# Kernel optimization log

Measured on AMD Instinct MI355X. Metric: run time of the kernel, lower is better.

## Reference

```python
import jax, jax.numpy as jnp
import numpy as np

B, S, D, H = 2, 2048, 1024, 16
DK = D // H


def setup_inputs() -> dict:
    key = jax.random.key(0)
    ks = jax.random.split(key, 8)
    scale = 1.0 / np.sqrt(D)
    inp = {
        "query": jax.random.normal(ks[0], (B, S, D), dtype=jnp.float32),
        "key": jax.random.normal(ks[1], (B, S, D), dtype=jnp.float32),
        "value": jax.random.normal(ks[2], (B, S, D), dtype=jnp.float32),
        # causal mask, broadcastable over batch and heads
        "mask": jnp.tril(jnp.ones((S, S), dtype=jnp.int32))[None, None, :, :],
        "W_q": jax.random.normal(ks[3], (D, D), dtype=jnp.float32) * scale,
        "W_k": jax.random.normal(ks[4], (D, D), dtype=jnp.float32) * scale,
        "W_v": jax.random.normal(ks[5], (D, D), dtype=jnp.float32) * scale,
        "W_o": jax.random.normal(ks[6], (D, D), dtype=jnp.float32) * scale,
    }
    return inp


def _split_heads(t):
    Bb, Ss, _ = t.shape
    return t.reshape(Bb, Ss, H, DK).transpose(0, 2, 1, 3)  # [B,H,S,DK]


def reference(query, key, value, mask, W_q, W_k, W_v, W_o):
    # Linear(d,d,bias=False): y = x @ W^T (torch stores weight as [out,in])
    Q = _split_heads(query @ W_q.T)
    K = _split_heads(key @ W_k.T)
    V = _split_heads(value @ W_v.T)
    scores = jnp.einsum("bhqd,bhkd->bhqk", Q, K) / jnp.sqrt(jnp.float32(DK))
    scores = jnp.where(mask == 0, -jnp.inf, scores)
    weights = jax.nn.softmax(scores, axis=-1)
    weights = jnp.nan_to_num(weights, nan=0.0)  # fully-masked rows -> 0
    # dropout is identity at inference
    x = jnp.einsum("bhqk,bhkd->bhqd", weights, V)
    x = x.transpose(0, 2, 1, 3).reshape(B, S, D)
    return x @ W_o.T
```

## Files before the change

### kernel.cpp

```cpp
#include <hip/hip_runtime.h>
#include <hip/hip_bf16.h>

#define D_MODEL 1024
#define NHEAD   16
#define HDK     64
#define SEQ     2048
#define BATCH   2
#define BS      (BATCH * SEQ)

typedef __attribute__((ext_vector_type(8))) short bf16x8;
typedef __attribute__((ext_vector_type(4))) float f32x4;

__device__ __forceinline__ unsigned short f2bf(float f) {
    unsigned u = __builtin_bit_cast(unsigned, f);
    u += 0x7fffu + ((u >> 16) & 1u);
    return (unsigned short)(u >> 16);
}

__device__ __forceinline__ unsigned pk_rne(float x, float y) {
    return (unsigned)f2bf(x) | ((unsigned)f2bf(y) << 16);
}

__device__ __forceinline__ unsigned pack_hi(float x, float y) {
    return __builtin_amdgcn_perm(__builtin_bit_cast(unsigned, y),
                                 __builtin_bit_cast(unsigned, x), 0x07060302u);
}

__device__ __forceinline__ float fexp2(float x) {
#if __has_builtin(__builtin_amdgcn_exp2f)
    return __builtin_amdgcn_exp2f(x);
#else
    return exp2f(x);
#endif
}

typedef const void __attribute__((address_space(1))) gas_void;
typedef void __attribute__((address_space(3))) las_void;

__device__ __forceinline__ void gll16(const void* g, void* l) {
    __builtin_amdgcn_global_load_lds((gas_void*)g, (las_void*)l, 16, 0, 0);
}

template <int ROWS>
__device__ __forceinline__ void stage_f32(const float* __restrict__ X, int ld,
                                          unsigned short* Ls, int t) {
    #pragma unroll
    for (int g = 0; g < ROWS / 32; ++g) {
        int row = (t >> 3) + g * 32;
        int sl  = t & 7;
        int col = (sl ^ (row & 7)) * 8;
        const float4* p = (const float4*)(X + (size_t)row * ld + col);
        float4 a = p[0], b = p[1];
        *(uint4*)&Ls[row * 64 + sl * 8] =
            make_uint4(pk_rne(a.x, a.y), pk_rne(a.z, a.w),
                       pk_rne(b.x, b.y), pk_rne(b.z, b.w));
    }
}

__global__ __launch_bounds__(256)
void proj_gemm(const float* __restrict__ qx, const float* __restrict__ kx,
               const float* __restrict__ vx, const float* __restrict__ wq,
               const float* __restrict__ wk, const float* __restrict__ wv,
               unsigned short* __restrict__ Qp, unsigned short* __restrict__ Kp,
               unsigned short* __restrict__ VT) {
    __shared__ __align__(16) unsigned short As[128 * 64];
    __shared__ __align__(16) unsigned short Bs[128 * 64];

    const int p = blockIdx.z;
    const float* X = p == 0 ? qx : p == 1 ? kx : vx;
    const float* W = p == 0 ? wq : p == 1 ? wk : wv;
    const int bm = blockIdx.y * 128, bn = blockIdx.x * 128;

    const int t    = threadIdx.x;
    const int w    = t >> 6;
    const int L    = t & 63;
    const int quad = L >> 4;
    const int lm   = L & 15;
    const int wr   = (w >> 1) * 64;
    const int wc   = (w & 1) * 64;

    f32x4 acc[4][4];
    #pragma unroll
    for (int ms = 0; ms < 4; ++ms)
        #pragma unroll
        for (int ns = 0; ns < 4; ++ns)
            acc[ms][ns] = (f32x4){0.f, 0.f, 0.f, 0.f};

    for (int kt = 0; kt < D_MODEL; kt += 64) {
        __syncthreads();
        stage_f32<128>(X + (size_t)bm * D_MODEL + kt, D_MODEL, As, t);
        stage_f32<128>(W + (size_t)bn * D_MODEL + kt, D_MODEL, Bs, t);
        __syncthreads();

        #pragma unroll
        for (int ch = 0; ch < 2; ++ch) {
            bf16x8 af[4], bfr[4];
            #pragma unroll
            for (int ms = 0; ms < 4; ++ms) {
                int row = wr + ms * 16 + lm;
                af[ms] = *(const bf16x8*)&As[row * 64 + (((ch * 4 + quad) ^ (row & 7)) * 8)];
            }
            #pragma unroll
            for (int ns = 0; ns < 4; ++ns) {
                int row = wc + ns * 16 + lm;
                bfr[ns] = *(const bf16x8*)&Bs[row * 64 + (((ch * 4 + quad) ^ (row & 7)) * 8)];
            }
            #pragma unroll
            for (int ms = 0; ms < 4; ++ms)
                #pragma unroll
                for (int ns = 0; ns < 4; ++ns)
                    acc[ms][ns] = __builtin_amdgcn_mfma_f32_16x16x32_bf16(
                        af[ms], bfr[ns], acc[ms][ns], 0, 0, 0);
        }
    }

    if (p == 2) {
        const int b    = bm >> 11;
        const int s_in = (bm & (SEQ - 1)) + wr;
        #pragma unroll
        for (int ms = 0; ms < 4; ++ms)
            #pragma unroll
            for (int ns = 0; ns < 4; ++ns) {
                int dg = bn + wc + ns * 16 + lm;
                int h  = dg >> 6, d = dg & 63;
                ushort4 pkv = make_ushort4(f2bf(acc[ms][ns][0]), f2bf(acc[ms][ns][1]),
                                           f2bf(acc[ms][ns][2]), f2bf(acc[ms][ns][3]));
                *(ushort4*)&VT[((size_t)((b * NHEAD + h) * HDK + d)) * SEQ +
                               s_in + ms * 16 + quad * 4] = pkv;
            }
    } else {
        unsigned short* Y = p == 0 ? Qp : Kp;
        const float scl = p == 0 ? 0.18033688011112042f : 1.0f;
        #pragma unroll
        for (int ms = 0; ms < 4; ++ms)
            #pragma unroll
            for (int ns = 0; ns < 4; ++ns)
                #pragma unroll
                for (int r = 0; r < 4; ++r)
                    Y[(size_t)(bm + wr + ms * 16 + quad * 4 + r) * D_MODEL +
                      bn + wc + ns * 16 + lm] = f2bf(acc[ms][ns][r] * scl);
    }
}

__global__ __launch_bounds__(256)
void out_gemm(const unsigned short* __restrict__ X, const float* __restrict__ W,
              float* __restrict__ Y) {
    __shared__ __align__(16) unsigned short As[128 * 64];
    __shared__ __align__(16) unsigned short Bs[64 * 64];
    const int bm = blockIdx.y * 128, bn = blockIdx.x * 64;

    const int t    = threadIdx.x;
    const int w    = t >> 6;
    const int L    = t & 63;
    const int quad = L >> 4;
    const int lm   = L & 15;
    const int r8   = L >> 3;
    const int sl   = L & 7;
    const int xcol = ((sl ^ r8) & 7) * 8;

    f32x4 acc[2][4];
    #pragma unroll
    for (int ms = 0; ms < 2; ++ms)
        #pragma unroll
        for (int ns = 0; ns < 4; ++ns)
            acc[ms][ns] = (f32x4){0.f, 0.f, 0.f, 0.f};

    for (int kt = 0; kt < D_MODEL; kt += 64) {
        __syncthreads();
        #pragma unroll
        for (int i = 0; i < 4; ++i) {
            int c = w * 4 + i;
            gll16(X + (size_t)(bm + c * 8 + r8) * D_MODEL + kt + xcol, &As[c * 512]);
        }
        stage_f32<64>(W + (size_t)bn * D_MODEL + kt, D_MODEL, Bs, t);
        __syncthreads();

        #pragma unroll
        for (int ch = 0; ch < 2; ++ch) {
            bf16x8 af[2], bfr[4];
            #pragma unroll
            for (int ms = 0; ms < 2; ++ms) {
                int row = w * 32 + ms * 16 + lm;
                af[ms] = *(const bf16x8*)&As[row * 64 + (((ch * 4 + quad) ^ (row & 7)) * 8)];
            }
            #pragma unroll
            for (int ns = 0; ns < 4; ++ns) {
                int row = ns * 16 + lm;
                bfr[ns] = *(const bf16x8*)&Bs[row * 64 + (((ch * 4 + quad) ^ (row & 7)) * 8)];
            }
            #pragma unroll
            for (int ms = 0; ms < 2; ++ms)
                #pragma unroll
                for (int ns = 0; ns < 4; ++ns)
                    acc[ms][ns] = __builtin_amdgcn_mfma_f32_16x16x32_bf16(
                        af[ms], bfr[ns], acc[ms][ns], 0, 0, 0);
        }
    }

    #pragma unroll
    for (int ms = 0; ms < 2; ++ms)
        #pragma unroll
        for (int ns = 0; ns < 4; ++ns)
            #pragma unroll
            for (int r = 0; r < 4; ++r)
                Y[(size_t)(bm + w * 32 + ms * 16 + quad * 4 + r) * D_MODEL +
                  bn + ns * 16 + lm] = acc[ms][ns][r];
}

__global__ __launch_bounds__(256)
void attn_mfma(const unsigned short* __restrict__ Q, const unsigned short* __restrict__ K,
               const unsigned short* __restrict__ VT, unsigned short* __restrict__ A) {
    __shared__ __align__(16) unsigned short Ks[2][64 * 72];
    __shared__ __align__(16) unsigned short Vs[2][64 * 72];
    __shared__ __align__(16) unsigned short Ps[4][16 * 72];

    const int t    = threadIdx.x;
    const int w    = t >> 6;
    const int L    = t & 63;
    const int quad = L >> 4;
    const int lm   = L & 15;

    const int f    = blockIdx.x;
    const int qt   = 31 - (f >> 5);
    const int bh   = f & 31;
    const int b    = bh >> 4, h = bh & 15;
    const int q0   = qt * 64;
    const size_t hb  = (size_t)b * SEQ * D_MODEL + h * HDK;
    const size_t vhb = (size_t)(b * NHEAD + h) * HDK;

    const int srow = t >> 2;
    const int sc   = (t & 3) * 16;
    const unsigned short* kp = K + hb + (size_t)srow * D_MODEL + sc;
    const unsigned short* vp = VT + (vhb + srow) * SEQ + sc;
    unsigned short* ps = &Ps[w][0];

    const int qrow = q0 + w * 16 + lm;
    bf16x8 Qf0, Qf1;
    {
        const unsigned short* qp = Q + hb + (size_t)qrow * D_MODEL + quad * 8;
        Qf0 = *(const bf16x8*)qp;
        Qf1 = *(const bf16x8*)(qp + 32);
    }

    f32x4 Oacc[4];
    #pragma unroll
    for (int nt = 0; nt < 4; ++nt) Oacc[nt] = (f32x4){0.f, 0.f, 0.f, 0.f};
    float m_run = -INFINITY, l_part = 0.f;

    float4 k0r = *(const float4*)kp;
    float4 k1r = *(const float4*)(kp + 8);
    float4 v0r = *(const float4*)vp;
    float4 v1r = *(const float4*)(vp + 8);
    *(float4*)&Ks[0][srow * 72 + sc]     = k0r;
    *(float4*)&Ks[0][srow * 72 + sc + 8] = k1r;
    *(float4*)&Vs[0][srow * 72 + sc]     = v0r;
    *(float4*)&Vs[0][srow * 72 + sc + 8] = v1r;
    if (qt >= 1) {
        k0r = *(const float4*)(kp + (size_t)64 * D_MODEL);
        k1r = *(const float4*)(kp + (size_t)64 * D_MODEL + 8);
        v0r = *(const float4*)(vp + 64);
        v1r = *(const float4*)(vp + 64 + 8);
    }
    __syncthreads();

    int bb = 0;
    for (int kt = 0; kt <= qt; ++kt) {
        if (kt < qt) {
            unsigned short* Kn = Ks[bb ^ 1];
            unsigned short* Vn = Vs[bb ^ 1];
            *(float4*)&Kn[srow * 72 + sc]     = k0r;
            *(float4*)&Kn[srow * 72 + sc + 8] = k1r;
            *(float4*)&Vn[srow * 72 + sc]     = v0r;
            *(float4*)&Vn[srow * 72 + sc + 8] = v1r;
            if (kt + 2 <= qt) {
                k0r = *(const float4*)(kp + (size_t)(kt + 2) * 64 * D_MODEL);
                k1r = *(const float4*)(kp + (size_t)(kt + 2) * 64 * D_MODEL + 8);
                v0r = *(const float4*)(vp + (kt + 2) * 64);
                v1r = *(const float4*)(vp + (kt + 2) * 64 + 8);
            }
        }
        const unsigned short* Kc = Ks[bb];
        const unsigned short* Vc = Vs[bb];

        f32x4 S[4];
        #pragma unroll
        for (int ct = 0; ct < 4; ++ct) {
            bf16x8 a0 = *(const bf16x8*)&Kc[(ct * 16 + lm) * 72 + quad * 8];
            bf16x8 a1 = *(const bf16x8*)&Kc[(ct * 16 + lm) * 72 + 32 + quad * 8];
            f32x4 z = (f32x4){0.f, 0.f, 0.f, 0.f};
            z = __builtin_amdgcn_mfma_f32_16x16x32_bf16(a0, Qf0, z, 0, 0, 0);
            z = __builtin_amdgcn_mfma_f32_16x16x32_bf16(a1, Qf1, z, 0, 0, 0);
            S[ct] = z;
        }

        if (kt == qt) {
            #pragma unroll
            for (int ct = 0; ct < 4; ++ct)
                #pragma unroll
                for (int r = 0; r < 4; ++r)
                    if ((q0 + ct * 16 + quad * 4 + r) > qrow)
                        S[ct][r] = -1e30f;
        }

        float m = fmaxf(fmaxf(fmaxf(S[0][0], S[0][1]), fmaxf(S[0][2], S[0][3])),
                        fmaxf(fmaxf(S[1][0], S[1][1]), fmaxf(S[1][2], S[1][3])));
        m = fmaxf(m, fmaxf(fmaxf(fmaxf(S[2][0], S[2][1]), fmaxf(S[2][2], S[2][3])),
                           fmaxf(fmaxf(S[3][0], S[3][1]), fmaxf(S[3][2], S[3][3]))));
        m = fmaxf(m, __shfl_xor(m, 16));
        m = fmaxf(m, __shfl_xor(m, 32));
        const float m_new = fmaxf(m_run, m);
        const float alpha = fexp2(m_run - m_new);
        m_run = m_new;
        float psum = 0.f;
        #pragma unroll
        for (int ct = 0; ct < 4; ++ct)
            #pragma unroll
            for (int r = 0; r < 4; ++r) {
                float e = fexp2(S[ct][r] - m_new);
                S[ct][r] = e;
                psum += e;
            }
        l_part = l_part * alpha + psum;

        #pragma unroll
        for (int ct = 0; ct < 4; ++ct) {
            uint2 pw = make_uint2(pack_hi(S[ct][0], S[ct][1]),
                                  pack_hi(S[ct][2], S[ct][3]));
            *(uint2*)&ps[lm * 72 + ct * 16 + quad * 4] = pw;
        }
        bf16x8 Pb0 = *(const bf16x8*)&ps[lm * 72 + quad * 8];
        bf16x8 Pb1 = *(const bf16x8*)&ps[lm * 72 + 32 + quad * 8];

        #pragma unroll
        for (int nt = 0; nt < 4; ++nt) {
            bf16x8 a0 = *(const bf16x8*)&Vc[(nt * 16 + lm) * 72 + quad * 8];
            bf16x8 a1 = *(const bf16x8*)&Vc[(nt * 16 + lm) * 72 + 32 + quad * 8];
            f32x4 o = Oacc[nt];
            #pragma unroll
            for (int r = 0; r < 4; ++r) o[r] *= alpha;
            o = __builtin_amdgcn_mfma_f32_16x16x32_bf16(a0, Pb0, o, 0, 0, 0);
            o = __builtin_amdgcn_mfma_f32_16x16x32_bf16(a1, Pb1, o, 0, 0, 0);
            Oacc[nt] = o;
        }

        __syncthreads();
        bb ^= 1;
    }

    float l = l_part;
    l += __shfl_xor(l, 16);
    l += __shfl_xor(l, 32);
    const float inv_l = 1.f / l;
    #pragma unroll
    for (int nt = 0; nt < 4; ++nt) {
        ushort4 pkv = make_ushort4(f2bf(Oacc[nt][0] * inv_l), f2bf(Oacc[nt][1] * inv_l),
                                   f2bf(Oacc[nt][2] * inv_l), f2bf(Oacc[nt][3] * inv_l));
        *(ushort4*)&ps[lm * 72 + nt * 16 + quad * 4] = pkv;
    }
    #pragma unroll
    for (int cc = 0; cc < 2; ++cc) {
        int row = cc * 8 + (L >> 3);
        int seg = L & 7;
        uint4 val = *(const uint4*)&ps[row * 72 + seg * 8];
        *(uint4*)&A[hb + (size_t)(q0 + w * 16 + row) * D_MODEL + seg * 8] = val;
    }
}

extern "C" void kernel_launch(void* const* d_in, const int* in_sizes, int n_in,
                              void* d_out, int out_size, void* d_ws, size_t ws_size,
                              hipStream_t stream) {
    const float* q  = (const float*)d_in[0];
    const float* k  = (const float*)d_in[1];
    const float* v  = (const float*)d_in[2];
    const float* Wq = (const float*)d_in[4];
    const float* Wk = (const float*)d_in[5];
    const float* Wv = (const float*)d_in[6];
    const float* Wo = (const float*)d_in[7];
    float* out = (float*)d_out;

    char* ws = (char*)d_ws;
    const size_t MB = 1024 * 1024;
    unsigned short* Qp  = (unsigned short*)(ws + 0 * MB);
    unsigned short* Kp  = (unsigned short*)(ws + 8 * MB);
    unsigned short* VTp = (unsigned short*)(ws + 16 * MB);
    unsigned short* Ap  = (unsigned short*)(ws + 24 * MB);

    proj_gemm<<<dim3(D_MODEL / 128, BS / 128, 3), 256, 0, stream>>>(
        q, k, v, Wq, Wk, Wv, Qp, Kp, VTp);

    attn_mfma<<<dim3(1024), 256, 0, stream>>>(Qp, Kp, VTp, Ap);

    out_gemm<<<dim3(D_MODEL / 64, BS / 128), 256, 0, stream>>>(Ap, Wo, out);
}
```

Before: 255.0 us.

## Pre-cast weights to bf16 and load them via direct-to-LDS; swizzle block order

Adds a kernel that converts all four weight matrices to bf16 once per call into workspace. The projection and output GEMMs then fetch weight tiles with global_load_lds instead of reading fp32 through registers and converting each time. Both GEMMs also move to a 1D grid with a grouped block-index mapping meant to improve L2 reuse. The cost is one extra launch plus an extra pass over the weights, and the workspace layout grows.

```diff
diff --git a/kernel.cpp b/kernel.cpp
--- a/kernel.cpp
+++ b/kernel.cpp
@@ -39,6 +39,20 @@
 
 __device__ __forceinline__ void gll16(const void* g, void* l) {
     __builtin_amdgcn_global_load_lds((gas_void*)g, (las_void*)l, 16, 0, 0);
+}
+
+__global__ __launch_bounds__(256)
+void cast_wt(const float* a, const float* b, const float* c, const float* dd,
+             unsigned short* oa, unsigned short* ob, unsigned short* oc,
+             unsigned short* od) {
+    int i = blockIdx.x * 256 + threadIdx.x;
+    const float* s = blockIdx.y == 0 ? a : blockIdx.y == 1 ? b : blockIdx.y == 2 ? c : dd;
+    unsigned short* d = blockIdx.y == 0 ? oa : blockIdx.y == 1 ? ob : blockIdx.y == 2 ? oc : od;
+    const float4* p = (const float4*)s + (size_t)i * 2;
+    float4 x = p[0], y = p[1];
+    uint4 pk = make_uint4(pk_rne(x.x, x.y), pk_rne(x.z, x.w),
+                          pk_rne(y.x, y.y), pk_rne(y.z, y.w));
+    *((uint4*)d + i) = pk;
 }
 
 template <int ROWS>
@@ -59,95 +73,21 @@
 
 __global__ __launch_bounds__(256)
 void proj_gemm(const float* __restrict__ qx, const float* __restrict__ kx,
-               const float* __restrict__ vx, const float* __restrict__ wq,
-               const float* __restrict__ wk, const float* __restrict__ wv,
+               const float* __restrict__ vx, const unsigned short* __restrict__ wq,
+               const unsigned short* __restrict__ wk, const unsigned short* __restrict__ wv,
                unsigned short* __restrict__ Qp, unsigned short* __restrict__ Kp,
                unsigned short* __restrict__ VT) {
     __shared__ __align__(16) unsigned short As[128 * 64];
     __shared__ __align__(16) unsigned short Bs[128 * 64];
 
-    const int p = blockIdx.z;
-    const float* X = p == 0 ? qx : p == 1 ? kx : vx;
-    const float* W = p == 0 ? wq : p == 1 ? wk : wv;
-    const int bm = blockIdx.y * 128, bn = blockIdx.x * 128;
-
-    const int t    = threadIdx.x;
-    const int w    = t >> 6;
-    const int L    = t & 63;
-    const int quad = L >> 4;
-    const int lm   = L & 15;
-    const int wr   = (w >> 1) * 64;
-    const int wc   = (w & 1) * 64;
-
-    f32x4 acc[4][4];
-    #pragma unroll
-    for (int ms = 0; ms < 4; ++ms)
-        #pragma unroll
-        for (int ns = 0; ns < 4; ++ns)
-            acc[ms][ns] = (f32x4){0.f, 0.f, 0.f, 0.f};
-
-    for (int kt = 0; kt < D_MODEL; kt += 64) {
-        __syncthreads();
-        stage_f32<128>(X + (size_t)bm * D_MODEL + kt, D_MODEL, As, t);
-        stage_f32<128>(W + (size_t)bn * D_MODEL + kt, D_MODEL, Bs, t);
-        __syncthreads();
-
-        #pragma unroll
-        for (int ch = 0; ch < 2; ++ch) {
-            bf16x8 af[4], bfr[4];
-            #pragma unroll
-            for (int ms = 0; ms < 4; ++ms) {
-                int row = wr + ms * 16 + lm;
-                af[ms] = *(const bf16x8*)&As[row * 64 + (((ch * 4 + quad) ^ (row & 7)) * 8)];
-            }
-            #pragma unroll
-            for (int ns = 0; ns < 4; ++ns) {
-                int row = wc + ns * 16 + lm;
-                bfr[ns] = *(const bf16x8*)&Bs[row * 64 + (((ch * 4 + quad) ^ (row & 7)) * 8)];
-            }
-            #pragma unroll
-            for (int ms = 0; ms < 4; ++ms)
-                #pragma unroll
-                for (int ns = 0; ns < 4; ++ns)
-                    acc[ms][ns] = __builtin_amdgcn_mfma_f32_16x16x32_bf16(
-                        af[ms], bfr[ns], acc[ms][ns], 0, 0, 0);
-        }
-    }
-
-    if (p == 2) {
-        const int b    = bm >> 11;
-        const int s_in = (bm & (SEQ - 1)) + wr;
-        #pragma unroll
-        for (int ms = 0; ms < 4; ++ms)
-            #pragma unroll
-            for (int ns = 0; ns < 4; ++ns) {
-                int dg = bn + wc + ns * 16 + lm;
-                int h  = dg >> 6, d = dg & 63;
-                ushort4 pkv = make_ushort4(f2bf(acc[ms][ns][0]), f2bf(acc[ms][ns][1]),
-                                           f2bf(acc[ms][ns][2]), f2bf(acc[ms][ns][3]));
-                *(ushort4*)&VT[((size_t)((b * NHEAD + h) * HDK + d)) * SEQ +
-                               s_in + ms * 16 + quad * 4] = pkv;
-            }
-    } else {
-        unsigned short* Y = p == 0 ? Qp : Kp;
-        const float scl = p == 0 ? 0.18033688011112042f : 1.0f;
-        #pragma unroll
-        for (int ms = 0; ms < 4; ++ms)
-            #pragma unroll
-            for (int ns = 0; ns < 4; ++ns)
-                #pragma unroll
-                for (int r = 0; r < 4; ++r)
-                    Y[(size_t)(bm + wr + ms * 16 + quad * 4 + r) * D_MODEL +
-                      bn + wc + ns * 16 + lm] = f2bf(acc[ms][ns][r] * scl);
-    }
-}
-
-__global__ __launch_bounds__(256)
-void out_gemm(const unsigned short* __restrict__ X, const float* __restrict__ W,
-              float* __restrict__ Y) {
-    __shared__ __align__(16) unsigned short As[128 * 64];
-    __shared__ __align__(16) unsigned short Bs[64 * 64];
-    const int bm = blockIdx.y * 128, bn = blockIdx.x * 64;
+    const int f  = blockIdx.x;
+    const int z  = f >> 8;
+    const int fl = f & 255;
+    const int bm = ((fl & 7) + 8 * (fl >> 6)) * 128;
+    const int bn = ((fl >> 3) & 7) * 128;
+
+    const float* X = z == 0 ? qx : z == 1 ? kx : vx;
+    const unsigned short* W = z == 0 ? wq : z == 1 ? wk : wv;
 
     const int t    = threadIdx.x;
     const int w    = t >> 6;
@@ -157,6 +97,94 @@
     const int r8   = L >> 3;
     const int sl   = L & 7;
     const int xcol = ((sl ^ r8) & 7) * 8;
+    const int wr   = (w >> 1) * 64;
+    const int wc   = (w & 1) * 64;
+
+    f32x4 acc[4][4];
+    #pragma unroll
+    for (int ms = 0; ms < 4; ++ms)
+        #pragma unroll
+        for (int ns = 0; ns < 4; ++ns)
+            acc[ms][ns] = (f32x4){0.f, 0.f, 0.f, 0.f};
+
+    for (int kt = 0; kt < D_MODEL; kt += 64) {
+        __syncthreads();
+        stage_f32<128>(X + (size_t)bm * D_MODEL + kt, D_MODEL, As, t);
+        #pragma unroll
+        for (int i = 0; i < 4; ++i) {
+            int c = w * 4 + i;
+            gll16(W + (size_t)(bn + c * 8 + r8) * D_MODEL + kt + xcol, &Bs[c * 512]);
+        }
+        __syncthreads();
+
+        #pragma unroll
+        for (int ch = 0; ch < 2; ++ch) {
+            bf16x8 af[4], bfr[4];
+            #pragma unroll
+            for (int ms = 0; ms < 4; ++ms) {
+                int row = wr + ms * 16 + lm;
+                af[ms] = *(const bf16x8*)&As[row * 64 + (((ch * 4 + quad) ^ (row & 7)) * 8)];
+            }
+            #pragma unroll
+            for (int ns = 0; ns < 4; ++ns) {
+                int row = wc + ns * 16 + lm;
+                bfr[ns] = *(const bf16x8*)&Bs[row * 64 + (((ch * 4 + quad) ^ (row & 7)) * 8)];
+            }
+            #pragma unroll
+            for (int ms = 0; ms < 4; ++ms)
+                #pragma unroll
+                for (int ns = 0; ns < 4; ++ns)
+                    acc[ms][ns] = __builtin_amdgcn_mfma_f32_16x16x32_bf16(
+                        af[ms], bfr[ns], acc[ms][ns], 0, 0, 0);
+        }
+    }
+
+    if (z == 2) {
+        const int b    = bm >> 11;
+        const int s_in = (bm & (SEQ - 1)) + wr;
+        #pragma unroll
+        for (int ms = 0; ms < 4; ++ms)
+            #pragma unroll
+            for (int ns = 0; ns < 4; ++ns) {
+                int dg = bn + wc + ns * 16 + lm;
+                int h  = dg >> 6, d = dg & 63;
+                ushort4 pkv = make_ushort4(f2bf(acc[ms][ns][0]), f2bf(acc[ms][ns][1]),
+                                           f2bf(acc[ms][ns][2]), f2bf(acc[ms][ns][3]));
+                *(ushort4*)&VT[((size_t)((b * NHEAD + h) * HDK + d)) * SEQ +
+                               s_in + ms * 16 + quad * 4] = pkv;
+            }
+    } else {
+        unsigned short* Y = z == 0 ? Qp : Kp;
+        const float scl = z == 0 ? 0.18033688011112042f : 1.0f;
+        #pragma unroll
+        for (int ms = 0; ms < 4; ++ms)
+            #pragma unroll
+            for (int ns = 0; ns < 4; ++ns)
+                #pragma unroll
+                for (int r = 0; r < 4; ++r)
+                    Y[(size_t)(bm + wr + ms * 16 + quad * 4 + r) * D_MODEL +
+                      bn + wc + ns * 16 + lm] = f2bf(acc[ms][ns][r] * scl);
+    }
+}
+
+__global__ __launch_bounds__(256)
+void out_gemm(const unsigned short* __restrict__ X, const unsigned short* __restrict__ W,
+              float* __restrict__ Y) {
+    __shared__ __align__(16) unsigned short As[128 * 64];
+    __shared__ __align__(16) unsigned short Bs[64 * 64];
+
+    const int f  = blockIdx.x;
+    const int bm = ((f & 7) + 8 * (f >> 7)) * 128;
+    const int bn = ((f >> 3) & 15) * 64;
+
+    const int t    = threadIdx.x;
+    const int w    = t >> 6;
+    const int L    = t & 63;
+    const int quad = L >> 4;
+    const int lm   = L & 15;
+    const int r8   = L >> 3;
+    const int sl   = L & 7;
+    const int xcol = ((sl ^ r8) & 7) * 8;
 
     f32x4 acc[2][4];
     #pragma unroll
@@ -172,7 +200,11 @@
             int c = w * 4 + i;
             gll16(X + (size_t)(bm + c * 8 + r8) * D_MODEL + kt + xcol, &As[c * 512]);
         }
-        stage_f32<64>(W + (size_t)bn * D_MODEL + kt, D_MODEL, Bs, t);
+        #pragma unroll
+        for (int i = 0; i < 2; ++i) {
+            int c = w * 2 + i;
+            gll16(W + (size_t)(bn + c * 8 + r8) * D_MODEL + kt + xcol, &Bs[c * 512]);
+        }
         __syncthreads();
 
         #pragma unroll
@@ -380,15 +412,22 @@
 
     char* ws = (char*)d_ws;
     const size_t MB = 1024 * 1024;
-    unsigned short* Qp  = (unsigned short*)(ws + 0 * MB);
-    unsigned short* Kp  = (unsigned short*)(ws + 8 * MB);
-    unsigned short* VTp = (unsigned short*)(ws + 16 * MB);
-    unsigned short* Ap  = (unsigned short*)(ws + 24 * MB);
-
-    proj_gemm<<<dim3(D_MODEL / 128, BS / 128, 3), 256, 0, stream>>>(
-        q, k, v, Wq, Wk, Wv, Qp, Kp, VTp);
+    unsigned short* wqb = (unsigned short*)(ws + 0 * MB);
+    unsigned short* wkb = (unsigned short*)(ws + 2 * MB);
+    unsigned short* wvb = (unsigned short*)(ws + 4 * MB);
+    unsigned short* wob = (unsigned short*)(ws + 6 * MB);
+    unsigned short* Qp  = (unsigned short*)(ws + 8 * MB);
+    unsigned short* Kp  = (unsigned short*)(ws + 16 * MB);
+    unsigned short* VTp = (unsigned short*)(ws + 24 * MB);
+    unsigned short* Ap  = (unsigned short*)(ws + 32 * MB);
+
+    const int nW8 = D_MODEL * D_MODEL / 8;
+    cast_wt<<<dim3(nW8 / 256, 4), 256, 0, stream>>>(
+        Wq, Wk, Wv, Wo, wqb, wkb, wvb, wob);
+
+    proj_gemm<<<dim3(768), 256, 0, stream>>>(q, k, v, wqb, wkb, wvb, Qp, Kp, VTp);
 
     attn_mfma<<<dim3(1024), 256, 0, stream>>>(Qp, Kp, VTp, Ap);
 
-    out_gemm<<<dim3(D_MODEL / 64, BS / 128), 256, 0, stream>>>(Ap, Wo, out);
-}
+    out_gemm<<<dim3(512), 256, 0, stream>>>(Ap, wob, out);
+}
```

New measurement: 235.2 us. -7.8%, faster.
